# Kernel tuning notes

Measured on AMD Instinct MI355X. Metric: run time of the kernel, lower is better.

Reference implementation:

```python
import jax, jax.numpy as jnp
import numpy as np
import math

B, C, H, W = 16, 384, 56, 56

def cos_map(N):
    # DCT-II basis matrix [freq n, spatial x], orthonormal
    wx = (jnp.arange(N, dtype=jnp.float32) + 0.5) / N
    wn = jnp.arange(N, dtype=jnp.float32)[:, None]
    w = jnp.cos(wn * wx[None, :] * jnp.pi) * math.sqrt(2.0 / N)
    return w.at[0, :].mul(1.0 / math.sqrt(2.0))

def setup_inputs() -> dict:
    key = jax.random.key(0)
    ks = jax.random.split(key, 14)
    s = 0.05  # weight scale for numerical sanity
    return {
        'x': jax.random.normal(ks[0], (B, C, H, W), jnp.float32),
        'freq_embed': jax.random.normal(ks[1], (B, H, W, C), jnp.float32),
        'dw_w': jax.random.normal(ks[2], (C, 1, 3, 3), jnp.float32) * s,
        'dw_b': jax.random.normal(ks[3], (C,), jnp.float32) * s,
        'lin_w': jax.random.normal(ks[4], (2 * C, C), jnp.float32) * s,
        'lin_b': jax.random.normal(ks[5], (2 * C,), jnp.float32) * s,
        'tok_w': jax.random.normal(ks[6], (C, C), jnp.float32) * s,
        'tok_b': jax.random.normal(ks[7], (C,), jnp.float32) * s,
        'ln_g': jnp.ones((C,), jnp.float32),
        'ln_b': jnp.zeros((C,), jnp.float32),
        'out_w': jax.random.normal(ks[8], (C, C), jnp.float32) * s,
        'out_b': jax.random.normal(ks[9], (C,), jnp.float32) * s,
        'c': jnp.ones((1,), jnp.float32),
        'alpha': jnp.full((1,), 0.1, jnp.float32),
    }

def reference(x, freq_embed, dw_w, dw_b, lin_w, lin_b, tok_w, tok_b, ln_g, ln_b, out_w, out_b, c, alpha):
    Bc, Cc, Hc, Wc = x.shape
    # depthwise 3x3 conv
    h = jax.lax.conv_general_dilated(
        x, dw_w, window_strides=(1, 1), padding=((1, 1), (1, 1)),
        dimension_numbers=('NCHW', 'OIHW', 'NCHW'), feature_group_count=Cc)
    h = h + dw_b[None, :, None, None]
    # linear to 2C, channel-last
    h = jnp.einsum('bchw,dc->bhwd', h, lin_w) + lin_b  # [B,H,W,2C]
    xx, z = jnp.split(h, 2, axis=-1)
    Wn = cos_map(Hc)  # [N,H]
    Wm = cos_map(Wc)  # [M,W]
    # DCT2D (x_u0 and x_v0 in the original are the identical transform)
    u = jnp.einsum('nh,bhwc->bnwc', Wn, xx)
    u = jnp.einsum('mw,bnwc->bnmc', Wm, u)  # [B,N,M,C]
    x_u0 = u
    x_v0 = u
    # trig wave-equation combination
    t = jax.nn.gelu(freq_embed @ tok_w.T + tok_b, approximate=False)
    c_t = c * t
    cos_t = jnp.cos(c_t)
    sin_t = jnp.sin(c_t) / (c + 1e-8)
    final = cos_t * x_u0 + sin_t * (x_v0 + 0.5 * alpha * x_u0)  # [B,N,M,C]
    # IDCT2D
    y = jnp.einsum('my,bnmc->bnyc', Wm, final)
    y = jnp.einsum('nx,bnyc->bxyc', Wn, y)  # [B,H,W,C]
    # LayerNorm over channels (eps=1e-5, biased variance)
    mu = y.mean(-1, keepdims=True)
    var = ((y - mu) ** 2).mean(-1, keepdims=True)
    yn = (y - mu) / jnp.sqrt(var + 1e-5) * ln_g + ln_b
    gate = jax.nn.silu(z)
    out = (yn * gate) @ out_w.T + out_b
    return out.transpose(0, 3, 1, 2)  # [B,C,H,W]
```

## Files before the change

kernel.cpp:

```cpp
#include <hip/hip_runtime.h>
#include <cstdint>
#include <cstddef>

typedef __attribute__((ext_vector_type(8))) short short8;
typedef __attribute__((ext_vector_type(4))) float floatx4;
typedef unsigned short u16;
typedef unsigned long long u64;

__device__ __forceinline__ float bf2f(u16 u) {
  union { unsigned int i; float f; } v; v.i = ((unsigned int)u) << 16; return v.f;
}
__device__ __forceinline__ u16 f2bf(float f) {
  union { float f; unsigned int u; } v; v.f = f;
  return (u16)((v.u + 0x7fffu + ((v.u >> 16) & 1u)) >> 16);
}
__device__ __forceinline__ void bfp(unsigned int p, float& x, float& y) {
  union { unsigned int i; float f; } a, b;
  a.i = p << 16; b.i = p & 0xffff0000u;
  x = a.f; y = b.f;
}
__device__ __forceinline__ unsigned int packbf(float a, float b) {
  return (unsigned int)f2bf(a) | ((unsigned int)f2bf(b) << 16);
}
__device__ __forceinline__ u64 pack4(float a, float b, float c, float d) {
  return (u64)f2bf(a) | ((u64)f2bf(b) << 16) | ((u64)f2bf(c) << 32) | ((u64)f2bf(d) << 48);
}

typedef __attribute__((address_space(1))) const unsigned int gu32;
typedef __attribute__((address_space(3))) unsigned int lu32;
__device__ __forceinline__ void gl2lds16(const void* g, void* l) {
  __builtin_amdgcn_global_load_lds((gu32*)g, (lu32*)l, 16, 0, 0);
}

__device__ __forceinline__ int xcd_swz(int id, int nwg) {
  int cpx = nwg >> 3;
  return (id & 7) * cpx + (id >> 3);
}

__device__ __forceinline__ float gelu_fast(float v) {
  float xg = v * 0.7071067811865476f;
  float ax = fabsf(xg);
  float tr = __builtin_amdgcn_rcpf(fmaf(0.3275911f, ax, 1.0f));
  float pl = tr * (0.254829592f + tr * (-0.284496736f + tr * (1.421413741f +
             tr * (-1.453152027f + tr * 1.061405429f))));
  float er = 1.0f - pl * __expf(-xg * xg);
  er = (xg < 0.f) ? -er : er;
  return 0.5f * v * (1.0f + er);
}

#define FE_F4 4816896
#define W_F4  147456
__global__ __launch_bounds__(256) void k_prep(const float* __restrict__ fe,
                                              const float* __restrict__ lw,
                                              const float* __restrict__ tw,
                                              const float* __restrict__ ow,
                                              u16* __restrict__ febf,
                                              u16* __restrict__ wbf,
                                              float* __restrict__ Wd) {
  int gid = blockIdx.x * 256 + threadIdx.x;
  if (gid < FE_F4) {
    float4 v = ((const float4*)fe)[gid];
    *(u64*)&febf[gid * 4] = pack4(v.x, v.y, v.z, v.w);
    return;
  }
  gid -= FE_F4;
  if (gid < W_F4) {
    const float* src; int off; int i = gid;
    if (i < 73728)        { src = lw; off = 0; }
    else if (i < 110592)  { src = tw; off = 294912; i -= 73728; }
    else                  { src = ow; off = 442368; i -= 110592; }
    float4 v = ((const float4*)src)[i];
    *(u64*)&wbf[off + i * 4] = pack4(v.x, v.y, v.z, v.w);
    return;
  }
  gid -= W_F4;
  if (gid < 784) {
    #pragma unroll
    for (int j = 0; j < 4; ++j) {
      int i = gid * 4 + j;
      int n = i / 56, x = i - n * 56;
      float v = cosf(3.14159265358979323846f * (float)n * ((float)x + 0.5f) / 56.0f)
                * 0.1889822365046136f;
      if (n == 0) v *= 0.7071067811865476f;
      Wd[i] = v;
    }
  }
}

__global__ __launch_bounds__(256) void k_conv(const float* __restrict__ x,
                                              const float* __restrict__ w9,
                                              const float* __restrict__ b1,
                                              u16* __restrict__ hbf) {
  __shared__ float xs[64 * 177];
  const int y = blockIdx.x, c0 = blockIdx.y * 64, b = blockIdx.z;
  const int tid = threadIdx.x, cl = tid & 63, wv = tid >> 6;
  float wr[9];
  #pragma unroll
  for (int k = 0; k < 9; ++k) wr[k] = w9[(c0 + cl) * 9 + k];
  const float br = b1[c0 + cl];
  for (int it = 0; it < 48; ++it) {
    int combo = it * 4 + wv;
    int c = combo / 3, r = combo - c * 3;
    int col = tid & 63;
    if (col < 58) {
      int gy = y + r - 1, gx = col - 1;
      float v = 0.f;
      if (gy >= 0 && gy < 56 && gx >= 0 && gx < 56)
        v = x[(((size_t)b * 384 + c0 + c) * 56 + gy) * 56 + gx];
      xs[c * 177 + r * 59 + col] = v;
    }
  }
  __syncthreads();
  for (int it = 0; it < 14; ++it) {
    int px = it * 4 + wv;
    float a = br;
    #pragma unroll
    for (int dy = 0; dy < 3; ++dy)
      #pragma unroll
      for (int dx = 0; dx < 3; ++dx)
        a += wr[dy * 3 + dx] * xs[cl * 177 + dy * 59 + px + dx];
    hbf[((size_t)b * 3136 + y * 56 + px) * 384 + c0 + cl] = f2bf(a);
  }
}

#define LDK 64
#define TS 132
#define S_U16 16896

__device__ __forceinline__ void stage_dma(const u16* __restrict__ src, int base, int kt,
                                          u16* __restrict__ buf, int tid) {
  const int r0 = tid >> 3, c8 = tid & 7;
  const int scol = (c8 ^ (r0 & 7)) << 3;
  #pragma unroll
  for (int p = 0; p < 4; ++p) {
    int row = p * 32 + r0;
    gl2lds16(src + (size_t)(base + row) * 384 + kt + scol, &buf[row * LDK + (c8 << 3)]);
  }
}

__device__ __forceinline__ short8 frag_read(const u16* buf, int r, int u) {
  return *(const short8*)&buf[r * LDK + (((u ^ (r & 7)) << 3))];
}

__device__ __forceinline__ void gemm_core(const u16* __restrict__ Ap,
                                          const u16* __restrict__ Bp,
                                          int m0, int n0, u16* As, u16* Bs,
                                          floatx4 acc[4][4]) {
  const int tid = threadIdx.x;
  const int lane = tid & 63, wv = tid >> 6;
  const int wm = wv & 1, wn = wv >> 1;
  const int q = lane >> 4, l15 = lane & 15;
  for (int kt = 0; kt < 384; kt += 64) {
    __syncthreads();
    stage_dma(Bp, n0, kt, Bs, tid);
    stage_dma(Ap, m0, kt, As, tid);
    __syncthreads();
    #pragma unroll
    for (int kc = 0; kc < 64; kc += 32) {
      short8 af[4], bf[4];
      #pragma unroll
      for (int i = 0; i < 4; ++i) {
        af[i] = frag_read(As, wm * 64 + i * 16 + l15, (kc >> 3) + q);
        bf[i] = frag_read(Bs, wn * 64 + i * 16 + l15, (kc >> 3) + q);
      }
      #pragma unroll
      for (int i = 0; i < 4; ++i)
        #pragma unroll
        for (int j = 0; j < 4; ++j)
          acc[i][j] = __builtin_amdgcn_mfma_f32_16x16x32_bf16(af[i], bf[j], acc[i][j], 0, 0, 0);
    }
  }
}

#define GEMM_PROLOGUE() \
  __shared__ __align__(16) u16 S[S_U16]; \
  u16* As = S; u16* Bs = S + 128 * LDK; \
  floatx4 acc[4][4]; \
  { floatx4 zv = {0.f, 0.f, 0.f, 0.f}; \
    _Pragma("unroll") for (int i = 0; i < 4; ++i) \
      _Pragma("unroll") for (int j = 0; j < 4; ++j) acc[i][j] = zv; } \
  const int tid = threadIdx.x; \
  const int lane = tid & 63, wv = tid >> 6; \
  const int wm = wv & 1, wn = wv >> 1, q = lane >> 4, l15 = lane & 15; \
  (void)lane;

__device__ __forceinline__ void tile_store(const u16* S, u16* dst, int m0) {
  const int tid = threadIdx.x;
  const int col = (tid & 31) * 4, rowo = tid >> 5;
  #pragma unroll
  for (int rr = 0; rr < 16; ++rr) {
    int row = rr * 8 + rowo;
    *(u64*)(dst + (size_t)(m0 + row) * 384 + col) = *(const u64*)&S[row * TS + col];
  }
}

__global__ __launch_bounds__(256) void k_gemm_lin(const u16* __restrict__ A,
                                                  const u16* __restrict__ Bw,
                                                  const float* __restrict__ bias,
                                                  u16* __restrict__ xx, u16* __restrict__ z) {
  GEMM_PROLOGUE();
  const int id = xcd_swz(blockIdx.x, 2352);
  const int n0 = (id % 6) * 128, m0 = (id / 6) * 128;
  gemm_core(A, Bw, m0, n0, As, Bs, acc);
  __syncthreads();
  #pragma unroll
  for (int i = 0; i < 4; ++i)
    #pragma unroll
    for (int j = 0; j < 4; ++j) {
      int nl = wn * 64 + j * 16 + l15;
      float bb = bias[n0 + nl];
      #pragma unroll
      for (int r = 0; r < 4; ++r) {
        int ml = wm * 64 + i * 16 + q * 4 + r;
        S[ml * TS + nl] = f2bf(acc[i][j][r] + bb);
      }
    }
  __syncthreads();
  u16* dst = (n0 < 384) ? (xx + n0) : (z + (n0 - 384));
  tile_store(S, dst, m0);
}

__global__ __launch_bounds__(256) void k_gemm_tok(const u16* __restrict__ A,
                                                  const u16* __restrict__ Bw,
                                                  const float* __restrict__ bias,
                                                  const float* __restrict__ cs,
                                                  const float* __restrict__ al,
                                                  u16* __restrict__ g) {
  GEMM_PROLOGUE();
  const int id = xcd_swz(blockIdx.x, 1176);
  const int n0 = (id % 3) * 128, m0 = (id / 3) * 128;
  gemm_core(A, Bw, m0, n0, As, Bs, acc);
  const float c0 = cs[0], a0 = al[0];
  const float sc = (1.0f / (c0 + 1e-8f)) * (1.0f + 0.5f * a0);
  __syncthreads();
  #pragma unroll
  for (int i = 0; i < 4; ++i)
    #pragma unroll
    for (int j = 0; j < 4; ++j) {
      int nl = wn * 64 + j * 16 + l15;
      float bb = bias[n0 + nl];
      #pragma unroll
      for (int r = 0; r < 4; ++r) {
        int ml = wm * 64 + i * 16 + q * 4 + r;
        float v = acc[i][j][r] + bb;
        float t = gelu_fast(v);
        float ct = c0 * t;
        S[ml * TS + nl] = f2bf(__cosf(ct) + __sinf(ct) * sc);
      }
    }
  __syncthreads();
  tile_store(S, g + n0, m0);
}

__global__ __launch_bounds__(256) void k_gemm_out(const u16* __restrict__ A,
                                                  const u16* __restrict__ Bp,
                                                  const float* __restrict__ bias,
                                                  float* __restrict__ outp) {
  GEMM_PROLOGUE();
  const int id = xcd_swz(blockIdx.x, 1176);
  const int m0 = (id % 3) * 128, n0 = (id / 3) * 128;
  gemm_core(A, Bp, m0, n0, As, Bs, acc);
  #pragma unroll
  for (int i = 0; i < 4; ++i)
    #pragma unroll
    for (int j = 0; j < 4; ++j) {
      int t = n0 + wn * 64 + j * 16 + l15;
      int b = t / 3136, p = t - b * 3136;
      #pragma unroll
      for (int r = 0; r < 4; ++r) {
        int m = m0 + wm * 64 + i * 16 + q * 4 + r;
        outp[((size_t)b * 384 + m) * 3136 + p] = acc[i][j][r] + bias[m];
      }
    }
}

__global__ __launch_bounds__(256) void k_dct_h(u16* __restrict__ xx,
                                               const float* __restrict__ Wd) {
  __shared__ float Xs[56 * 128];
  __shared__ float Ws[3136];
  const int w = blockIdx.x, cb = blockIdx.y * 128, b = blockIdx.z;
  const int tid = threadIdx.x;
  for (int i = tid; i < 3136; i += 256) Ws[i] = Wd[i];
  for (int i = tid; i < 56 * 64; i += 256) {
    int h = i >> 6, cu = i & 63;
    unsigned int p = *(const unsigned int*)(xx + ((size_t)(b * 56 + h) * 56 + w) * 384 + cb + cu * 2);
    bfp(p, Xs[h * 128 + cu * 2], Xs[h * 128 + cu * 2 + 1]);
  }
  __syncthreads();
  const int lane = tid & 63, wv = tid >> 6;
  float a0[14], a1[14];
  #pragma unroll
  for (int k = 0; k < 14; ++k) { a0[k] = 0.f; a1[k] = 0.f; }
  for (int h = 0; h < 56; ++h) {
    float x0 = Xs[h * 128 + 2 * lane];
    float x1 = Xs[h * 128 + 2 * lane + 1];
    #pragma unroll
    for (int k = 0; k < 14; ++k) {
      float wn = Ws[(wv + 4 * k) * 56 + h];
      a0[k] += wn * x0; a1[k] += wn * x1;
    }
  }
  #pragma unroll
  for (int k = 0; k < 14; ++k) {
    int n = wv + 4 * k;
    *(unsigned int*)(xx + ((size_t)(b * 56 + n) * 56 + w) * 384 + cb + 2 * lane) = packbf(a0[k], a1[k]);
  }
}

__global__ __launch_bounds__(256) void k_mid(u16* __restrict__ u1,
                                             const u16* __restrict__ g,
                                             const float* __restrict__ Wd) {
  __shared__ float Us[56 * 64];
  __shared__ float Vs[56 * 64];
  __shared__ float Ws[3136];
  const int n = blockIdx.x, cb = blockIdx.y * 64, b = blockIdx.z;
  const int tid = threadIdx.x;
  for (int i = tid; i < 3136; i += 256) Ws[i] = Wd[i];
  for (int i = tid; i < 56 * 32; i += 256) {
    int ww = i >> 5, cu = i & 31;
    unsigned int p = *(const unsigned int*)(u1 + ((size_t)(b * 56 + n) * 56 + ww) * 384 + cb + cu * 2);
    bfp(p, Us[ww * 64 + cu * 2], Us[ww * 64 + cu * 2 + 1]);
  }
  __syncthreads();
  const int lane = tid & 63, wv = tid >> 6;
  {
    float a[14];
    #pragma unroll
    for (int k = 0; k < 14; ++k) a[k] = 0.f;
    for (int ww = 0; ww < 56; ++ww) {
      float xv = Us[ww * 64 + lane];
      #pragma unroll
      for (int k = 0; k < 14; ++k)
        a[k] += Ws[(wv + 4 * k) * 56 + ww] * xv;
    }
    #pragma unroll
    for (int k = 0; k < 14; ++k) Vs[(wv + 4 * k) * 64 + lane] = a[k];
  }
  __syncthreads();
  for (int i = tid; i < 56 * 32; i += 256) {
    int m = i >> 5, cu = i & 31;
    unsigned int p = *(const unsigned int*)(g + ((size_t)(b * 56 + n) * 56 + m) * 384 + cb + cu * 2);
    float g0, g1; bfp(p, g0, g1);
    Vs[m * 64 + cu * 2]     *= g0;
    Vs[m * 64 + cu * 2 + 1] *= g1;
  }
  __syncthreads();
  {
    float a[14];
    #pragma unroll
    for (int k = 0; k < 14; ++k) a[k] = 0.f;
    for (int m = 0; m < 56; ++m) {
      float xv = Vs[m * 64 + lane];
      #pragma unroll
      for (int k = 0; k < 14; ++k)
        a[k] += Ws[m * 56 + (wv + 4 * k)] * xv;
    }
    #pragma unroll
    for (int k = 0; k < 14; ++k) {
      int yy = wv + 4 * k;
      u1[((size_t)(b * 56 + n) * 56 + yy) * 384 + cb + lane] = f2bf(a[k]);
    }
  }
}

__global__ __launch_bounds__(256) void k_idct_h(u16* __restrict__ y1,
                                                const float* __restrict__ Wd) {
  __shared__ float Ys[56 * 128];
  __shared__ float Ws[3136];
  const int yy = blockIdx.x, cb = blockIdx.y * 128, b = blockIdx.z;
  const int tid = threadIdx.x;
  for (int i = tid; i < 3136; i += 256) Ws[i] = Wd[i];
  for (int i = tid; i < 56 * 64; i += 256) {
    int nn = i >> 6, cu = i & 63;
    unsigned int p = *(const unsigned int*)(y1 + ((size_t)(b * 56 + nn) * 56 + yy) * 384 + cb + cu * 2);
    bfp(p, Ys[nn * 128 + cu * 2], Ys[nn * 128 + cu * 2 + 1]);
  }
  __syncthreads();
  const int lane = tid & 63, wv = tid >> 6;
  float a0[14], a1[14];
  #pragma unroll
  for (int k = 0; k < 14; ++k) { a0[k] = 0.f; a1[k] = 0.f; }
  for (int nn = 0; nn < 56; ++nn) {
    float x0 = Ys[nn * 128 + 2 * lane];
    float x1 = Ys[nn * 128 + 2 * lane + 1];
    #pragma unroll
    for (int k = 0; k < 14; ++k) {
      float wn = Ws[nn * 56 + (wv + 4 * k)];
      a0[k] += wn * x0; a1[k] += wn * x1;
    }
  }
  #pragma unroll
  for (int k = 0; k < 14; ++k) {
    int x = wv + 4 * k;
    *(unsigned int*)(y1 + ((size_t)(b * 56 + x) * 56 + yy) * 384 + cb + 2 * lane) = packbf(a0[k], a1[k]);
  }
}

__global__ __launch_bounds__(256) void k_ln(u16* __restrict__ y2,
                                            const u16* __restrict__ z,
                                            const float* __restrict__ lgm,
                                            const float* __restrict__ lbt) {
  const int t = blockIdx.x * 4 + (threadIdx.x >> 6);
  const int lane = threadIdx.x & 63;
  u16* yr = y2 + (size_t)t * 384;
  const u16* zr = z + (size_t)t * 384;
  float v[6]; float s = 0.f, s2 = 0.f;
  #pragma unroll
  for (int k = 0; k < 3; ++k) {
    unsigned int p = *(const unsigned int*)(yr + 2 * lane + 128 * k);
    float f0, f1; bfp(p, f0, f1);
    v[2 * k] = f0; v[2 * k + 1] = f1;
    s += f0 + f1; s2 += f0 * f0 + f1 * f1;
  }
  #pragma unroll
  for (int off = 32; off >= 1; off >>= 1) {
    s  += __shfl_xor(s, off, 64);
    s2 += __shfl_xor(s2, off, 64);
  }
  const float mu  = s * (1.0f / 384.0f);
  const float var = s2 * (1.0f / 384.0f) - mu * mu;
  const float inv = rsqrtf(var + 1e-5f);
  #pragma unroll
  for (int k = 0; k < 3; ++k) {
    int c = 2 * lane + 128 * k;
    float z0, z1;
    bfp(*(const unsigned int*)(zr + c), z0, z1);
    float yn0 = (v[2 * k]     - mu) * inv * lgm[c]     + lbt[c];
    float yn1 = (v[2 * k + 1] - mu) * inv * lgm[c + 1] + lbt[c + 1];
    float ga0 = z0 / (1.0f + __expf(-z0));
    float ga1 = z1 / (1.0f + __expf(-z1));
    *(unsigned int*)(yr + c) = packbf(yn0 * ga0, yn1 * ga1);
  }
}

extern "C" void kernel_launch(void* const* d_in, const int* in_sizes, int n_in,
                              void* d_out, int out_size, void* d_ws, size_t ws_size,
                              hipStream_t stream) {
  const float* x     = (const float*)d_in[0];
  const float* fe    = (const float*)d_in[1];
  const float* dw_w  = (const float*)d_in[2];
  const float* dw_b  = (const float*)d_in[3];
  const float* lin_w = (const float*)d_in[4];
  const float* lin_b = (const float*)d_in[5];
  const float* tok_w = (const float*)d_in[6];
  const float* tok_b = (const float*)d_in[7];
  const float* ln_g  = (const float*)d_in[8];
  const float* ln_b  = (const float*)d_in[9];
  const float* out_w = (const float*)d_in[10];
  const float* out_b = (const float*)d_in[11];
  const float* cs    = (const float*)d_in[12];
  const float* al    = (const float*)d_in[13];
  float* outp = (float*)d_out;
  char* ws = (char*)d_ws;

  float* Wd = (float*)(ws + 0);
  u16* SA = (u16*)(ws + 16384);
  u16* SB = (u16*)(ws + 16384 + 38535168);
  u16* SC = (u16*)(ws + 16384 + 2 * (size_t)38535168);
  u16* Wbf = (u16*)(ws + 16384 + 3 * (size_t)38535168);
  u16* FEbf = (u16*)d_out;

  k_prep<<<dim3(19396), dim3(256), 0, stream>>>(fe, lin_w, tok_w, out_w, FEbf, Wbf, Wd);
  k_conv<<<dim3(56, 6, 16), dim3(256), 0, stream>>>(x, dw_w, dw_b, SA);
  k_gemm_lin<<<dim3(2352), dim3(256), 0, stream>>>(SA, Wbf, lin_b, SB, SC);
  k_gemm_tok<<<dim3(1176), dim3(256), 0, stream>>>(FEbf, Wbf + 294912, tok_b, cs, al, SA);
  k_dct_h<<<dim3(56, 3, 16), dim3(256), 0, stream>>>(SB, Wd);
  k_mid<<<dim3(56, 6, 16), dim3(256), 0, stream>>>(SB, SA, Wd);
  k_idct_h<<<dim3(56, 3, 16), dim3(256), 0, stream>>>(SB, Wd);
  k_ln<<<dim3(12544), dim3(256), 0, stream>>>(SB, SC, ln_g, ln_b);
  k_gemm_out<<<dim3(1176), dim3(256), 0, stream>>>(Wbf + 442368, SB, out_b, outp);
}
```

Before: 753.1 us.

## Retile depthwise conv to 4 rows x 32 channels with sliding register window

```diff
diff --git a/kernel.cpp b/kernel.cpp
--- a/kernel.cpp
+++ b/kernel.cpp
@@ -91,35 +91,54 @@
                                               const float* __restrict__ w9,
                                               const float* __restrict__ b1,
                                               u16* __restrict__ hbf) {
-  __shared__ float xs[64 * 177];
-  const int y = blockIdx.x, c0 = blockIdx.y * 64, b = blockIdx.z;
-  const int tid = threadIdx.x, cl = tid & 63, wv = tid >> 6;
+  __shared__ float xsr[33 + 6 * 60 * 33];
+  float* xs = xsr + 33;
+  const int y0 = blockIdx.x * 4, c0 = blockIdx.y * 32, b = blockIdx.z;
+  const int tid = threadIdx.x;
+  for (int i = tid; i < 33; i += 256) xsr[i] = 0.f;
+  for (int i = tid; i < 792; i += 256) {
+    int row = i / 132, j = i - row * 132;
+    xs[(row * 60 + 56) * 33 + j] = 0.f;
+  }
+  for (int i = tid; i < 2688; i += 256) {
+    int ch = i / 84, rem = i - ch * 84;
+    int row = rem / 14, q4 = rem - row * 14;
+    int gy = y0 + row - 1;
+    float4 v = {0.f, 0.f, 0.f, 0.f};
+    if (gy >= 0 && gy < 56)
+      v = *(const float4*)(x + ((size_t)(b * 384 + c0 + ch) * 56 + gy) * 56 + q4 * 4);
+    int base = (row * 60 + q4 * 4) * 33 + ch;
+    xs[base] = v.x; xs[base + 33] = v.y; xs[base + 66] = v.z; xs[base + 99] = v.w;
+  }
+  __syncthreads();
+  const int ch = tid & 31, g = tid >> 5;
+  const int r = g & 3, pxb = (g >> 2) * 28;
   float wr[9];
   #pragma unroll
-  for (int k = 0; k < 9; ++k) wr[k] = w9[(c0 + cl) * 9 + k];
-  const float br = b1[c0 + cl];
-  for (int it = 0; it < 48; ++it) {
-    int combo = it * 4 + wv;
-    int c = combo / 3, r = combo - c * 3;
-    int col = tid & 63;
-    if (col < 58) {
-      int gy = y + r - 1, gx = col - 1;
-      float v = 0.f;
-      if (gy >= 0 && gy < 56 && gx >= 0 && gx < 56)
-        v = x[(((size_t)b * 384 + c0 + c) * 56 + gy) * 56 + gx];
-      xs[c * 177 + r * 59 + col] = v;
-    }
-  }
-  __syncthreads();
-  for (int it = 0; it < 14; ++it) {
-    int px = it * 4 + wv;
+  for (int k = 0; k < 9; ++k) wr[k] = w9[(c0 + ch) * 9 + k];
+  const float br = b1[c0 + ch];
+  float p0[3], p1[3];
+  #pragma unroll
+  for (int dy = 0; dy < 3; ++dy) {
+    p0[dy] = xs[((r + dy) * 60 + pxb - 1) * 33 + ch];
+    p1[dy] = xs[((r + dy) * 60 + pxb) * 33 + ch];
+  }
+  u16* orow = hbf + ((size_t)b * 3136 + (y0 + r) * 56) * 384 + c0 + ch;
+  #pragma unroll 4
+  for (int px = pxb; px < pxb + 28; ++px) {
+    float p2[3];
+    #pragma unroll
+    for (int dy = 0; dy < 3; ++dy) p2[dy] = xs[((r + dy) * 60 + px + 1) * 33 + ch];
     float a = br;
     #pragma unroll
-    for (int dy = 0; dy < 3; ++dy)
-      #pragma unroll
-      for (int dx = 0; dx < 3; ++dx)
-        a += wr[dy * 3 + dx] * xs[cl * 177 + dy * 59 + px + dx];
-    hbf[((size_t)b * 3136 + y * 56 + px) * 384 + c0 + cl] = f2bf(a);
+    for (int dy = 0; dy < 3; ++dy) {
+      a += wr[dy * 3 + 0] * p0[dy];
+      a += wr[dy * 3 + 1] * p1[dy];
+      a += wr[dy * 3 + 2] * p2[dy];
+    }
+    orow[(size_t)px * 384] = f2bf(a);
+    #pragma unroll
+    for (int dy = 0; dy < 3; ++dy) { p0[dy] = p1[dy]; p1[dy] = p2[dy]; }
   }
 }
 
@@ -461,7 +480,7 @@
   u16* FEbf = (u16*)d_out;
 
   k_prep<<<dim3(19396), dim3(256), 0, stream>>>(fe, lin_w, tok_w, out_w, FEbf, Wbf, Wd);
-  k_conv<<<dim3(56, 6, 16), dim3(256), 0, stream>>>(x, dw_w, dw_b, SA);
+  k_conv<<<dim3(14, 12, 16), dim3(256), 0, stream>>>(x, dw_w, dw_b, SA);
   k_gemm_lin<<<dim3(2352), dim3(256), 0, stream>>>(SA, Wbf, lin_b, SB, SC);
   k_gemm_tok<<<dim3(1176), dim3(256), 0, stream>>>(FEbf, Wbf + 294912, tok_b, cs, al, SA);
   k_dct_h<<<dim3(56, 3, 16), dim3(256), 0, stream>>>(SB, Wd);
```

Result: faster. 622.8 us (-17.3%).
